# Kernel optimization log

Measured on AMD Instinct MI355X. Metric: run time of the kernel, lower is better.

Reference implementation:

```python
import jax, jax.numpy as jnp
import numpy as np

N_NODES = 20000
N_EDGES = 600000
HIDDEN = 128
OUT = 128
EPS = 0.0  # GINConv default eps, not trainable by default


def _mlp(x, W1, b1, W2, b2):
    h = jax.nn.relu(x @ W1 + b1)
    return jax.nn.relu(h @ W2 + b2)


def _gin_conv(x, edge_index, W1, b1, W2, b2):
    src, dst = edge_index[0], edge_index[1]
    # scatter-add neighbor aggregation: agg[dst] += x[src]
    agg = jax.ops.segment_sum(x[src], dst, num_segments=N_NODES)
    return _mlp((1.0 + EPS) * x + agg, W1, b1, W2, b2)


def _forward_once(x, edge_index, params):
    (W11, b11, W12, b12, W21, b21, W22, b22, Wf, bf) = params
    x = _gin_conv(x, edge_index, W11, b11, W12, b12)
    x = _gin_conv(x, edge_index, W21, b21, W22, b22)
    g = jnp.sum(x, axis=0)  # sum-pool over nodes -> [HIDDEN]
    return g @ Wf + bf


def setup_inputs() -> dict:
    key = jax.random.key(0)
    ks = jax.random.split(key, 16)
    def lin(k, fan_in, fan_out):
        kw, kb = jax.random.split(k)
        bound = 1.0 / np.sqrt(fan_in)
        W = jax.random.uniform(kw, (fan_in, fan_out), jnp.float32, -bound, bound)
        b = jax.random.uniform(kb, (fan_out,), jnp.float32, -bound, bound)
        return W, b
    W11, b11 = lin(ks[0], 1, HIDDEN)
    W12, b12 = lin(ks[1], HIDDEN, HIDDEN)
    W21, b21 = lin(ks[2], HIDDEN, HIDDEN)
    W22, b22 = lin(ks[3], HIDDEN, HIDDEN)
    Wf, bf = lin(ks[4], HIDDEN, OUT)
    inp = {
        "x_a": jax.random.normal(ks[5], (N_NODES, 1), jnp.float32),
        "edge_index_a": jax.random.randint(ks[6], (2, N_EDGES), 0, N_NODES, jnp.int64 if jax.config.jax_enable_x64 else jnp.int32),
        "x_p": jax.random.normal(ks[7], (N_NODES, 1), jnp.float32),
        "edge_index_p": jax.random.randint(ks[8], (2, N_EDGES), 0, N_NODES, jnp.int64 if jax.config.jax_enable_x64 else jnp.int32),
        "x_n": jax.random.normal(ks[9], (N_NODES, 1), jnp.float32),
        "edge_index_n": jax.random.randint(ks[10], (2, N_EDGES), 0, N_NODES, jnp.int64 if jax.config.jax_enable_x64 else jnp.int32),
        "W11": W11, "b11": b11, "W12": W12, "b12": b12,
        "W21": W21, "b21": b21, "W22": W22, "b22": b22,
        "Wf": Wf, "bf": bf,
    }
    return inp


def reference(x_a, edge_index_a, x_p, edge_index_p, x_n, edge_index_n,
              W11, b11, W12, b12, W21, b21, W22, b22, Wf, bf):
    params = (W11, b11, W12, b12, W21, b21, W22, b22, Wf, bf)
    a = _forward_once(x_a, edge_index_a, params)
    p = _forward_once(x_p, edge_index_p, params)
    n = _forward_once(x_n, edge_index_n, params)
    return (a, p, n)
```

## Files before the change

### kernel.cpp

```cpp
#include <hip/hip_runtime.h>

#define N_NODES 20000
#define N_EDGES 600000
#define HID 128
#define NB N_NODES
#define NBP (NB + 8)
#define NBLK64 313
#define BPG 160
#define CHUNK (N_EDGES / BPG)
#define NBUCK 157
#define BSH 7
#define COLCAP 760832

typedef unsigned int uint32;
typedef __attribute__((ext_vector_type(8))) short bf16x8v;
typedef __attribute__((ext_vector_type(4))) float f32x4;
typedef __attribute__((ext_vector_type(2))) float f32x2;

#define P_OFF     0
#define BCNT_OFF  1800000
#define BBASE_OFF 1875360
#define X1_OFF    1875840
#define H2_OFF    5717376
#define COL_OFF   9557376
#define RPE_OFF   11839872
#define GSUM_OFF  11959872
#define TS_OFF    11960256
#define UV_OFF    11960384
#define W21P_OFF  11993408
#define W22P_OFF  12001600

static __device__ inline unsigned short f2bf(float f) {
    uint32 u = __float_as_uint(f);
    return (unsigned short)((u + 0x7fffu + ((u >> 16) & 1u)) >> 16);
}
static __device__ inline uint32 pack2(float a, float b) {
    return (uint32)f2bf(a) | ((uint32)f2bf(b) << 16);
}
static __device__ inline f32x2 unpk(uint32 v) {
    f32x2 r;
    r.x = __uint_as_float(v << 16);
    r.y = __uint_as_float(v & 0xffff0000u);
    return r;
}

__launch_bounds__(256)
__global__ void prep2_kernel(const float* __restrict__ W11, const float* __restrict__ b11,
                             const float* __restrict__ W12, const float* __restrict__ b12,
                             const float* __restrict__ W21, const float* __restrict__ W22,
                             float* __restrict__ ts, float* __restrict__ UV,
                             uint32* __restrict__ W21p, uint32* __restrict__ W22p,
                             float* __restrict__ gsum) {
    int blk = blockIdx.x, tid = threadIdx.x;
    if (blk < 8) {
        __shared__ float w12s[128][16];
        __shared__ float du[128][16];
        __shared__ float dv[128][16];
        __shared__ float pu[16][16], pv[16][16];
        __shared__ float bu[16][16], bv[16][16];
        __shared__ float wsh[128], bsh[128], tss[128], tsh[128];
        __shared__ int osh[128];
        int c0 = blk * 16;
        if (tid < 128) {
            float w = W11[tid], b = b11[tid];
            wsh[tid] = w; bsh[tid] = b;
            tsh[tid] = (w != 0.0f) ? (-b / w) : 3.0e38f;
        }
        {
            int r0 = tid >> 4, cc2 = tid & 15;
            for (int r = r0; r < 128; r += 16)
                w12s[r][cc2] = W12[r * HID + c0 + cc2];
        }
        __syncthreads();
        if (tid < 128) {
            float t = tsh[tid];
            int rank = 0;
            for (int j = 0; j < 128; ++j) {
                float tj = tsh[j];
                if (tj < t || (tj == t && j < tid)) ++rank;
            }
            tss[rank] = t; osh[rank] = tid;
        }
        __syncthreads();
        if (blk == 0 && tid < 128) ts[tid] = tss[tid];
        int c = tid & 15, t = tid >> 4;
        float su = 0.f, sv = 0.f;
#pragma unroll
        for (int m = 0; m < 8; ++m) {
            int j = t * 8 + m;
            int k = osh[j];
            float wk = wsh[k], bk = bsh[k], w12 = w12s[k][c];
            float sg = (wk > 0.f) ? 1.f : ((wk < 0.f) ? -1.f : 0.f);
            du[j][c] = sg * wk * w12;
            dv[j][c] = sg * bk * w12;
            float wb = wsh[j], bb = bsh[j], w12b = w12s[j][c];
            if (wb < 0.f)                     { su += wb * w12b; sv += bb * w12b; }
            else if (wb == 0.f && bb > 0.f)   { sv += bb * w12b; }
        }
        bu[t][c] = su; bv[t][c] = sv;
        __syncthreads();
        float ru = 0.f, rv = 0.f;
#pragma unroll
        for (int m = 0; m < 8; ++m) {
            int j = t * 8 + m;
            ru += du[j][c]; du[j][c] = ru;
            rv += dv[j][c]; dv[j][c] = rv;
        }
        pu[t][c] = ru; pv[t][c] = rv;
        __syncthreads();
        if (t == 0) {
            float baseu = 0.f;
            float basev = b12[c0 + c];
            for (int q = 0; q < 16; ++q) { baseu += bu[q][c]; basev += bv[q][c]; }
            float ou = baseu, ov = basev;
            for (int q = 0; q < 16; ++q) {
                float tu = pu[q][c], tv = pv[q][c];
                pu[q][c] = ou; pv[q][c] = ov;
                ou += tu; ov += tv;
            }
            UV[c0 + c] = baseu; UV[128 + c0 + c] = basev;
        }
        __syncthreads();
        float offu = pu[t][c], offv = pv[t][c];
#pragma unroll
        for (int m = 0; m < 8; ++m) {
            int j = t * 8 + m;
            UV[(j + 1) * 256 + c0 + c]       = offu + du[j][c];
            UV[(j + 1) * 256 + 128 + c0 + c] = offv + dv[j][c];
        }
    } else {
        int idx = (blk - 8) * 256 + tid;
        int tt = idx >> 9, c = (idx >> 6) & 7, l = idx & 63;
        int kbase = tt * 32 + (l >> 4) * 8;
        int colv = c * 16 + (l & 15);
#pragma unroll
        for (int jw = 0; jw < 4; ++jw) {
            float f0 = W21[(kbase + 2 * jw) * HID + colv];
            float f1 = W21[(kbase + 2 * jw + 1) * HID + colv];
            W21p[idx * 4 + jw] = pack2(f0, f1);
            f0 = W22[(kbase + 2 * jw) * HID + colv];
            f1 = W22[(kbase + 2 * jw + 1) * HID + colv];
            W22p[idx * 4 + jw] = pack2(f0, f1);
        }
        if (blk == 8)
            for (int i = tid; i < 384; i += 256) gsum[i] = 0.0f;
    }
}

__launch_bounds__(512)
__global__ void bhist_kernel(const int* __restrict__ ea, const int* __restrict__ ep,
                             const int* __restrict__ en, uint32* __restrict__ bcnt) {
    __shared__ uint32 c[NBUCK];
    int g = blockIdx.y, blk = blockIdx.x, tid = threadIdx.x;
    const int* e = (g == 0) ? ea : (g == 1) ? ep : en;
    if (tid < NBUCK) c[tid] = 0;
    __syncthreads();
    int base = blk * CHUNK;
    for (int i = tid; i < CHUNK; i += 512)
        atomicAdd(&c[e[N_EDGES + base + i] >> BSH], 1u);
    __syncthreads();
    if (tid < NBUCK) bcnt[((size_t)g * BPG + blk) * NBUCK + tid] = c[tid];
}

__launch_bounds__(256)
__global__ void bscan_kernel(uint32* __restrict__ bcnt, uint32* __restrict__ bbase) {
    __shared__ uint32 btot[NBUCK];
    int g = blockIdx.x, tid = threadIdx.x;
    if (tid < NBUCK) {
        uint32 run = 0;
        for (int blk = 0; blk < BPG; ++blk) {
            size_t idx = ((size_t)g * BPG + blk) * NBUCK + tid;
            uint32 t = bcnt[idx];
            bcnt[idx] = run;
            run += t;
        }
        btot[tid] = run;
    }
    __syncthreads();
    if (tid == 0) {
        uint32 run = 0;
        for (int k = 0; k < NBUCK; ++k) { bbase[g * 158 + k] = run; run += btot[k]; }
        bbase[g * 158 + NBUCK] = run;
    }
}

__launch_bounds__(512)
__global__ void bpart_kernel(const int* __restrict__ ea, const int* __restrict__ ep,
                             const int* __restrict__ en, const uint32* __restrict__ bcnt,
                             const uint32* __restrict__ bbase, uint32* __restrict__ P) {
    __shared__ uint32 cur[NBUCK];
    int g = blockIdx.y, blk = blockIdx.x, tid = threadIdx.x;
    const int* e = (g == 0) ? ea : (g == 1) ? ep : en;
    if (tid < NBUCK)
        cur[tid] = bbase[g * 158 + tid] + bcnt[((size_t)g * BPG + blk) * NBUCK + tid];
    __syncthreads();
    int base = blk * CHUNK;
    uint32* Pg = P + (size_t)g * N_EDGES;
    for (int i = tid; i < CHUNK; i += 512) {
        int src = e[base + i];
        int dst = e[N_EDGES + base + i];
        uint32 pos = atomicAdd(&cur[dst >> BSH], 1u);
        Pg[pos] = (uint32)src | ((uint32)(dst & 127) << 16);
    }
}

__launch_bounds__(256)
__global__ void bcsr_l1_kernel(const uint32* __restrict__ bbase, const uint32* __restrict__ P,
                               const float* __restrict__ xa, const float* __restrict__ xp,
                               const float* __restrict__ xn,
                               const float* __restrict__ ts, const float* __restrict__ UV,
                               int* __restrict__ rpe, uint32* __restrict__ col,
                               uint32* __restrict__ X1) {
    __shared__ uint32 h[128];
    __shared__ uint32 hraw[128];
    __shared__ uint32 pls[128];
    __shared__ uint32 wendS;
    __shared__ float accs[128];
    __shared__ float tsh[128];
    __shared__ int pat[128];
    int k = blockIdx.x, g = blockIdx.y, tid = threadIdx.x;
    const float* x = (g == 0) ? xa : (g == 1) ? xp : xn;
    int beg = (int)bbase[g * 158 + k], end = (int)bbase[g * 158 + k + 1];
    int size = end - beg;
    int wbase = beg + k * 1024;
    int n0 = k * 128;
    int cnt_nodes = NB - n0; if (cnt_nodes > 128) cnt_nodes = 128;
    const uint32 ZOFFB = (uint32)NB << 8;
    if (tid < 128) { h[tid] = 0; accs[tid] = 0.0f; tsh[tid] = ts[tid]; }
    __syncthreads();
    const uint32* Pg = P + (size_t)g * N_EDGES + beg;
    for (int i = tid; i < size; i += 256)
        atomicAdd(&h[(Pg[i] >> 16) & 127], 1u);
    __syncthreads();
    if (tid == 0) {
        uint32 run = 0;
        for (int d = 0; d < 128; ++d) {
            hraw[d] = h[d];
            pls[d] = run;
            run += (h[d] + 8u) & ~7u;
        }
        wendS = (uint32)wbase + run;
    }
    __syncthreads();
    uint32* colg = col + (size_t)g * COLCAP;
    if (tid < cnt_nodes) {
        int node = n0 + tid;
        rpe[((size_t)g * NB + node) * 2]     = wbase + (int)pls[tid];
        rpe[((size_t)g * NB + node) * 2 + 1] = wbase + (int)(pls[tid] + ((hraw[tid] + 8u) & ~7u));
        colg[wbase + pls[tid]] = (uint32)node << 8;
        uint32 e0 = pls[tid] + 1u + hraw[tid];
        uint32 e1 = pls[tid] + ((hraw[tid] + 8u) & ~7u);
        for (uint32 q = e0; q < e1; ++q) colg[wbase + q] = ZOFFB;
    } else if (tid < 128) {
        uint32 e0 = pls[tid];
        uint32 e1 = pls[tid] + 8u;
        for (uint32 q = e0; q < e1; ++q) colg[wbase + q] = ZOFFB;
    }
    if (tid < 128) h[tid] = pls[tid] + 1u;
    __syncthreads();
    for (int i = tid; i < size; i += 256) {
        uint32 w = Pg[i];
        int d = (w >> 16) & 127;
        int src = (int)(w & 0xffffu);
        uint32 r = atomicAdd(&h[d], 1u);
        colg[wbase + r] = (uint32)src << 8;
        atomicAdd(&accs[d], x[src]);
    }
    if (k == 0 && tid < 64)
        *((uint32*)&X1[((size_t)g * NBP + NB) * 64] + tid) = 0u;
    if (k == NBUCK - 1 && tid < 64)
        colg[wendS + tid] = ZOFFB;
    __syncthreads();
    if (tid < cnt_nodes) {
        float s = accs[tid] + x[n0 + tid];
        int lo = 0, hi = 128;
        while (lo < hi) { int mid = (lo + hi) >> 1; if (tsh[mid] < s) lo = mid + 1; else hi = mid; }
        pat[tid] = lo;
        accs[tid] = s;
    }
    __syncthreads();
    uint32* X1g = X1 + ((size_t)g * NBP + n0) * 64;
#pragma unroll 4
    for (int it = 0; it < 32; ++it) {
        int idx = it * 256 + tid;
        int d = idx >> 6, w = idx & 63;
        if (d < cnt_nodes) {
            const float* Up = UV + (size_t)pat[d] * 256;
            float s = accs[d];
            float2 u = *(const float2*)&Up[w * 2];
            float2 v = *(const float2*)&Up[128 + w * 2];
            float r0 = fmaxf(fmaf(s, u.x, v.x), 0.0f);
            float r1 = fmaxf(fmaf(s, u.y, v.y), 0.0f);
            X1g[(size_t)d * 64 + w] = pack2(r0, r1);
        }
    }
}

__launch_bounds__(256)
__global__ void gather2_kernel(const int* __restrict__ rpe, const uint32* __restrict__ col,
                               const uint32* __restrict__ X1, uint32* __restrict__ H2) {
    int b = blockIdx.x;
    int xcd = b & 7, s = b >> 3;
    int phase = s / 313, slot = s - phase * 313;
    const int gt[3][2] = {{0, 1}, {2, 2}, {0, 1}};
    const int ht[3][2] = {{0, 0}, {0, 1}, {1, 1}};
    int g = gt[phase][xcd >> 2];
    int h = ht[phase][xcd >> 2];
    int nb = slot * 4 + (xcd & 3);
    if (nb >= 1250) return;
    int tid = threadIdx.x;
    int wave = tid >> 6, lane = tid & 63;
    int node = nb * 16 + wave * 4 + (lane >> 4);
    int l4 = lane & 15;
    int sl = l4 >> 3;
    int w = l4 & 7;
    const uint32* colg = col + (size_t)g * COLCAP;
    int2 be = *(const int2*)&rpe[((size_t)g * NB + node) * 2];
    int beg = be.x, end = be.y;
    const char* Bg = (const char*)(X1 + (size_t)g * NBP * 64) + h * 128 + w * 16;
    f32x2 A0 = {0.f, 0.f}, A1 = {0.f, 0.f}, A2 = {0.f, 0.f}, A3 = {0.f, 0.f};
    uint32 ca = colg[beg + sl];
    uint32 cb = colg[beg + 2 + sl];
    uint32 cc = colg[beg + 4 + sl];
    uint32 cd = colg[beg + 6 + sl];
    for (int j = beg; j < end; j += 8) {
        uint32 c0 = ca, c1 = cb, c2 = cc, c3 = cd;
        ca = colg[j + 8 + sl];
        cb = colg[j + 10 + sl];
        cc = colg[j + 12 + sl];
        cd = colg[j + 14 + sl];
        uint4 v0 = *(const uint4*)(Bg + c0);
        uint4 v1 = *(const uint4*)(Bg + c1);
        uint4 v2 = *(const uint4*)(Bg + c2);
        uint4 v3 = *(const uint4*)(Bg + c3);
        A0 += unpk(v0.x); A1 += unpk(v0.y); A2 += unpk(v0.z); A3 += unpk(v0.w);
        A0 += unpk(v1.x); A1 += unpk(v1.y); A2 += unpk(v1.z); A3 += unpk(v1.w);
        A0 += unpk(v2.x); A1 += unpk(v2.y); A2 += unpk(v2.z); A3 += unpk(v2.w);
        A0 += unpk(v3.x); A1 += unpk(v3.y); A2 += unpk(v3.z); A3 += unpk(v3.w);
    }
    float a0 = A0.x, a1 = A0.y, a2 = A1.x, a3 = A1.y;
    float a4 = A2.x, a5 = A2.y, a6 = A3.x, a7 = A3.y;
    a0 += __shfl_xor(a0, 8);
    a1 += __shfl_xor(a1, 8);
    a2 += __shfl_xor(a2, 8);
    a3 += __shfl_xor(a3, 8);
    a4 += __shfl_xor(a4, 8);
    a5 += __shfl_xor(a5, 8);
    a6 += __shfl_xor(a6, 8);
    a7 += __shfl_xor(a7, 8);
    if (sl == 0) {
        uint4 o;
        o.x = pack2(a0, a1); o.y = pack2(a2, a3);
        o.z = pack2(a4, a5); o.w = pack2(a6, a7);
        *(uint4*)&H2[(size_t)(g * NB + node) * 64 + h * 32 + w * 4] = o;
    }
}

__launch_bounds__(256)
__global__ void mlp2_kernel(const uint32* __restrict__ H2,
                            const uint32* __restrict__ W21p, const float* __restrict__ b21,
                            const uint32* __restrict__ W22p, const float* __restrict__ b22,
                            float* __restrict__ gsum) {
    __shared__ uint32 tl[64 * 64];
    __shared__ float psum[HID];
    int g = blockIdx.y;
    int base = blockIdx.x * 64;
    int nvalid = NB - base; if (nvalid > 64) nvalid = 64;
    int tid = threadIdx.x;
    int wave = tid >> 6, l = tid & 63;
    int lq = l >> 4, lr = l & 15;
    if (tid < HID) psum[tid] = 0.0f;
    __syncthreads();

    f32x4 acc[8];
#pragma unroll
    for (int c = 0; c < 8; ++c) acc[c] = (f32x4){0.f, 0.f, 0.f, 0.f};
    int arow = wave * 16 + lr;
    int arowc = (arow < nvalid) ? arow : 0;
    const uint32* h2row = H2 + ((size_t)g * NB + base + arowc) * 64;
#pragma unroll
    for (int t = 0; t < 4; ++t) {
        uint4 av = *(const uint4*)&h2row[t * 16 + lq * 4];
        bf16x8v af = __builtin_bit_cast(bf16x8v, av);
#pragma unroll
        for (int c = 0; c < 8; ++c) {
            uint4 bv = *(const uint4*)&W21p[((t * 8 + c) * 64 + l) * 4];
            acc[c] = __builtin_amdgcn_mfma_f32_16x16x32_bf16(
                af, __builtin_bit_cast(bf16x8v, bv), acc[c], 0, 0, 0);
        }
    }
    unsigned short* tls = (unsigned short*)tl;
#pragma unroll
    for (int c = 0; c < 8; ++c) {
        int colv = c * 16 + lr;
        float bb = b21[colv];
#pragma unroll
        for (int q = 0; q < 4; ++q) {
            int row = wave * 16 + lq * 4 + q;
            float v = fmaxf(acc[c][q] + bb, 0.0f);
            int byte = row * 256 + ((colv * 2) ^ ((row & 7) << 4));
            tls[byte >> 1] = f2bf(v);
        }
    }
    f32x4 acc2[8];
#pragma unroll
    for (int c = 0; c < 8; ++c) acc2[c] = (f32x4){0.f, 0.f, 0.f, 0.f};
#pragma unroll
    for (int t = 0; t < 4; ++t) {
        int rbyte = arow * 256 + (((t * 64 + lq * 16)) ^ ((arow & 7) << 4));
        uint4 av = *(const uint4*)((const char*)tl + rbyte);
        bf16x8v af = __builtin_bit_cast(bf16x8v, av);
#pragma unroll
        for (int c = 0; c < 8; ++c) {
            uint4 bv = *(const uint4*)&W22p[((t * 8 + c) * 64 + l) * 4];
            acc2[c] = __builtin_amdgcn_mfma_f32_16x16x32_bf16(
                af, __builtin_bit_cast(bf16x8v, bv), acc2[c], 0, 0, 0);
        }
    }
#pragma unroll
    for (int c = 0; c < 8; ++c) {
        float bb = b22[c * 16 + lr];
        float s = 0.0f;
#pragma unroll
        for (int q = 0; q < 4; ++q) {
            int row = wave * 16 + lq * 4 + q;
            float v = fmaxf(acc2[c][q] + bb, 0.0f);
            s += (row < nvalid) ? v : 0.0f;
        }
        s += __shfl_xor(s, 16);
        s += __shfl_xor(s, 32);
        if (lq == 0) atomicAdd(&psum[c * 16 + lr], s);
    }
    __syncthreads();
    if (tid < HID) atomicAdd(&gsum[g * HID + tid], psum[tid]);
}

__global__ void final_kernel(const float* __restrict__ gsum, const float* __restrict__ Wf,
                             const float* __restrict__ bf, float* __restrict__ out) {
    int tid = threadIdx.x;
    int g = tid >> 7;
    int o = tid & 127;
    float acc = bf[o];
    for (int k = 0; k < HID; ++k)
        acc += gsum[g * HID + k] * Wf[k * HID + o];
    out[g * HID + o] = acc;
}

extern "C" void kernel_launch(void* const* d_in, const int* in_sizes, int n_in,
                              void* d_out, int out_size, void* d_ws, size_t ws_size,
                              hipStream_t stream) {
    const float* xa = (const float*)d_in[0];
    const int*   ea = (const int*)d_in[1];
    const float* xp = (const float*)d_in[2];
    const int*   ep = (const int*)d_in[3];
    const float* xn = (const float*)d_in[4];
    const int*   en = (const int*)d_in[5];
    const float* W11 = (const float*)d_in[6];
    const float* b11 = (const float*)d_in[7];
    const float* W12 = (const float*)d_in[8];
    const float* b12 = (const float*)d_in[9];
    const float* W21 = (const float*)d_in[10];
    const float* b21 = (const float*)d_in[11];
    const float* W22 = (const float*)d_in[12];
    const float* b22 = (const float*)d_in[13];
    const float* Wf  = (const float*)d_in[14];
    const float* bf  = (const float*)d_in[15];

    float*  ws    = (float*)d_ws;
    uint32* P     = (uint32*)(ws + P_OFF);
    uint32* bcnt  = (uint32*)(ws + BCNT_OFF);
    uint32* bbase = (uint32*)(ws + BBASE_OFF);
    uint32* X1    = (uint32*)(ws + X1_OFF);
    uint32* H2    = (uint32*)(ws + H2_OFF);
    uint32* col   = (uint32*)(ws + COL_OFF);
    int*    rpe   = (int*)(ws + RPE_OFF);
    float*  gsum  = ws + GSUM_OFF;
    float*  ts    = ws + TS_OFF;
    float*  UV    = ws + UV_OFF;
    uint32* W21p  = (uint32*)(ws + W21P_OFF);
    uint32* W22p  = (uint32*)(ws + W22P_OFF);
    float*  out   = (float*)d_out;

    prep2_kernel<<<16, 256, 0, stream>>>(W11, b11, W12, b12, W21, W22, ts, UV, W21p, W22p, gsum);
    bhist_kernel<<<dim3(BPG, 3), 512, 0, stream>>>(ea, ep, en, bcnt);
    bscan_kernel<<<3, 256, 0, stream>>>(bcnt, bbase);
    bpart_kernel<<<dim3(BPG, 3), 512, 0, stream>>>(ea, ep, en, bcnt, bbase, P);
    bcsr_l1_kernel<<<dim3(NBUCK, 3), 256, 0, stream>>>(bbase, P, xa, xp, xn, ts, UV, rpe, col, X1);
    gather2_kernel<<<7512, 256, 0, stream>>>(rpe, col, X1, H2);
    mlp2_kernel<<<dim3(NBLK64, 3), 256, 0, stream>>>(H2, W21p, b21, W22p, b22, gsum);
    final_kernel<<<1, 384, 0, stream>>>(gsum, Wf, bf, out);
}
```

Before: 133.1 us.

## Merge prep into histogram kernel and fold bucket scan into partition kernel

The weight-prep work now runs as extra blocks inside the bucket-histogram launch. The separate scan kernel is removed: every partition block recomputes its own prefix offsets and the bucket totals from the histogram counts. This cuts the launch count from eight to six and removes two serial launch gaps. In exchange, each of the 480 partition blocks re-reads all 160 count rows for its graph, and the prep blocks carry a larger 512-thread shape in which half the threads sit idle.

```diff
diff --git a/kernel.cpp b/kernel.cpp
--- a/kernel.cpp
+++ b/kernel.cpp
@@ -44,15 +44,32 @@
     return r;
 }
 
-__launch_bounds__(256)
-__global__ void prep2_kernel(const float* __restrict__ W11, const float* __restrict__ b11,
-                             const float* __restrict__ W12, const float* __restrict__ b12,
-                             const float* __restrict__ W21, const float* __restrict__ W22,
-                             float* __restrict__ ts, float* __restrict__ UV,
-                             uint32* __restrict__ W21p, uint32* __restrict__ W22p,
-                             float* __restrict__ gsum) {
-    int blk = blockIdx.x, tid = threadIdx.x;
-    if (blk < 8) {
+__launch_bounds__(512)
+__global__ void bhist_prep_kernel(const int* __restrict__ ea, const int* __restrict__ ep,
+                                  const int* __restrict__ en, uint32* __restrict__ bcnt,
+                                  const float* __restrict__ W11, const float* __restrict__ b11,
+                                  const float* __restrict__ W12, const float* __restrict__ b12,
+                                  const float* __restrict__ W21, const float* __restrict__ W22,
+                                  float* __restrict__ ts, float* __restrict__ UV,
+                                  uint32* __restrict__ W21p, uint32* __restrict__ W22p,
+                                  float* __restrict__ gsum) {
+    int tid = threadIdx.x;
+    if (blockIdx.x < BPG) {
+        __shared__ uint32 c[NBUCK];
+        int g = blockIdx.y, blk = blockIdx.x;
+        const int* e = (g == 0) ? ea : (g == 1) ? ep : en;
+        if (tid < NBUCK) c[tid] = 0;
+        __syncthreads();
+        int base = blk * CHUNK;
+        for (int i = tid; i < CHUNK; i += 512)
+            atomicAdd(&c[e[N_EDGES + base + i] >> BSH], 1u);
+        __syncthreads();
+        if (tid < NBUCK) bcnt[((size_t)g * BPG + blk) * NBUCK + tid] = c[tid];
+        return;
+    }
+    int p = (blockIdx.x - BPG) * 3 + blockIdx.y;
+    if (p >= 16) return;
+    if (p < 8) {
         __shared__ float w12s[128][16];
         __shared__ float du[128][16];
         __shared__ float dv[128][16];
@@ -60,7 +77,7 @@
         __shared__ float bu[16][16], bv[16][16];
         __shared__ float wsh[128], bsh[128], tss[128], tsh[128];
         __shared__ int osh[128];
-        int c0 = blk * 16;
+        int c0 = p * 16;
         if (tid < 128) {
             float w = W11[tid], b = b11[tid];
             wsh[tid] = w; bsh[tid] = b;
@@ -68,7 +85,7 @@
         }
         {
             int r0 = tid >> 4, cc2 = tid & 15;
-            for (int r = r0; r < 128; r += 16)
+            for (int r = r0; r < 128; r += 32)
                 w12s[r][cc2] = W12[r * HID + c0 + cc2];
         }
         __syncthreads();
@@ -82,31 +99,35 @@
             tss[rank] = t; osh[rank] = tid;
         }
         __syncthreads();
-        if (blk == 0 && tid < 128) ts[tid] = tss[tid];
+        if (p == 0 && tid < 128) ts[tid] = tss[tid];
         int c = tid & 15, t = tid >> 4;
-        float su = 0.f, sv = 0.f;
-#pragma unroll
-        for (int m = 0; m < 8; ++m) {
-            int j = t * 8 + m;
-            int k = osh[j];
-            float wk = wsh[k], bk = bsh[k], w12 = w12s[k][c];
-            float sg = (wk > 0.f) ? 1.f : ((wk < 0.f) ? -1.f : 0.f);
-            du[j][c] = sg * wk * w12;
-            dv[j][c] = sg * bk * w12;
-            float wb = wsh[j], bb = bsh[j], w12b = w12s[j][c];
-            if (wb < 0.f)                     { su += wb * w12b; sv += bb * w12b; }
-            else if (wb == 0.f && bb > 0.f)   { sv += bb * w12b; }
-        }
-        bu[t][c] = su; bv[t][c] = sv;
-        __syncthreads();
-        float ru = 0.f, rv = 0.f;
-#pragma unroll
-        for (int m = 0; m < 8; ++m) {
-            int j = t * 8 + m;
-            ru += du[j][c]; du[j][c] = ru;
-            rv += dv[j][c]; dv[j][c] = rv;
-        }
-        pu[t][c] = ru; pv[t][c] = rv;
+        if (t < 16) {
+            float su = 0.f, sv = 0.f;
+#pragma unroll
+            for (int m = 0; m < 8; ++m) {
+                int j = t * 8 + m;
+                int k = osh[j];
+                float wk = wsh[k], bk = bsh[k], w12 = w12s[k][c];
+                float sg = (wk > 0.f) ? 1.f : ((wk < 0.f) ? -1.f : 0.f);
+                du[j][c] = sg * wk * w12;
+                dv[j][c] = sg * bk * w12;
+                float wb = wsh[j], bb = bsh[j], w12b = w12s[j][c];
+                if (wb < 0.f)                     { su += wb * w12b; sv += bb * w12b; }
+                else if (wb == 0.f && bb > 0.f)   { sv += bb * w12b; }
+            }
+            bu[t][c] = su; bv[t][c] = sv;
+        }
+        __syncthreads();
+        if (t < 16) {
+            float ru = 0.f, rv = 0.f;
+#pragma unroll
+            for (int m = 0; m < 8; ++m) {
+                int j = t * 8 + m;
+                ru += du[j][c]; du[j][c] = ru;
+                rv += dv[j][c]; dv[j][c] = rv;
+            }
+            pu[t][c] = ru; pv[t][c] = rv;
+        }
         __syncthreads();
         if (t == 0) {
             float baseu = 0.f;
@@ -121,15 +142,17 @@
             UV[c0 + c] = baseu; UV[128 + c0 + c] = basev;
         }
         __syncthreads();
-        float offu = pu[t][c], offv = pv[t][c];
-#pragma unroll
-        for (int m = 0; m < 8; ++m) {
-            int j = t * 8 + m;
-            UV[(j + 1) * 256 + c0 + c]       = offu + du[j][c];
-            UV[(j + 1) * 256 + 128 + c0 + c] = offv + dv[j][c];
-        }
-    } else {
-        int idx = (blk - 8) * 256 + tid;
+        if (t < 16) {
+            float offu = pu[t][c], offv = pv[t][c];
+#pragma unroll
+            for (int m = 0; m < 8; ++m) {
+                int j = t * 8 + m;
+                UV[(j + 1) * 256 + c0 + c]       = offu + du[j][c];
+                UV[(j + 1) * 256 + 128 + c0 + c] = offv + dv[j][c];
+            }
+        }
+    } else if (tid < 256) {
+        int idx = (p - 8) * 256 + tid;
         int tt = idx >> 9, c = (idx >> 6) & 7, l = idx & 63;
         int kbase = tt * 32 + (l >> 4) * 8;
         int colv = c * 16 + (l & 15);
@@ -142,57 +165,40 @@
             f1 = W22[(kbase + 2 * jw + 1) * HID + colv];
             W22p[idx * 4 + jw] = pack2(f0, f1);
         }
-        if (blk == 8)
+        if (p == 8)
             for (int i = tid; i < 384; i += 256) gsum[i] = 0.0f;
-    }
-}
-
-__launch_bounds__(512)
-__global__ void bhist_kernel(const int* __restrict__ ea, const int* __restrict__ ep,
-                             const int* __restrict__ en, uint32* __restrict__ bcnt) {
-    __shared__ uint32 c[NBUCK];
-    int g = blockIdx.y, blk = blockIdx.x, tid = threadIdx.x;
-    const int* e = (g == 0) ? ea : (g == 1) ? ep : en;
-    if (tid < NBUCK) c[tid] = 0;
-    __syncthreads();
-    int base = blk * CHUNK;
-    for (int i = tid; i < CHUNK; i += 512)
-        atomicAdd(&c[e[N_EDGES + base + i] >> BSH], 1u);
-    __syncthreads();
-    if (tid < NBUCK) bcnt[((size_t)g * BPG + blk) * NBUCK + tid] = c[tid];
-}
-
-__launch_bounds__(256)
-__global__ void bscan_kernel(uint32* __restrict__ bcnt, uint32* __restrict__ bbase) {
-    __shared__ uint32 btot[NBUCK];
-    int g = blockIdx.x, tid = threadIdx.x;
-    if (tid < NBUCK) {
-        uint32 run = 0;
-        for (int blk = 0; blk < BPG; ++blk) {
-            size_t idx = ((size_t)g * BPG + blk) * NBUCK + tid;
-            uint32 t = bcnt[idx];
-            bcnt[idx] = run;
-            run += t;
-        }
-        btot[tid] = run;
-    }
-    __syncthreads();
-    if (tid == 0) {
-        uint32 run = 0;
-        for (int k = 0; k < NBUCK; ++k) { bbase[g * 158 + k] = run; run += btot[k]; }
-        bbase[g * 158 + NBUCK] = run;
     }
 }
 
 __launch_bounds__(512)
 __global__ void bpart_kernel(const int* __restrict__ ea, const int* __restrict__ ep,
                              const int* __restrict__ en, const uint32* __restrict__ bcnt,
-                             const uint32* __restrict__ bbase, uint32* __restrict__ P) {
+                             uint32* __restrict__ bbase, uint32* __restrict__ P) {
     __shared__ uint32 cur[NBUCK];
+    __shared__ uint32 totS[NBUCK];
+    __shared__ uint32 sbase[NBUCK + 1];
     int g = blockIdx.y, blk = blockIdx.x, tid = threadIdx.x;
     const int* e = (g == 0) ? ea : (g == 1) ? ep : en;
-    if (tid < NBUCK)
-        cur[tid] = bbase[g * 158 + tid] + bcnt[((size_t)g * BPG + blk) * NBUCK + tid];
+    if (tid < NBUCK) {
+        uint32 myoff = 0, tot = 0;
+        const uint32* bc = bcnt + (size_t)g * BPG * NBUCK + tid;
+        for (int k = 0; k < BPG; ++k) {
+            uint32 v = bc[(size_t)k * NBUCK];
+            if (k < blk) myoff += v;
+            tot += v;
+        }
+        cur[tid] = myoff;
+        totS[tid] = tot;
+    }
+    __syncthreads();
+    if (tid == 0) {
+        uint32 run = 0;
+        for (int b2 = 0; b2 < NBUCK; ++b2) { sbase[b2] = run; run += totS[b2]; }
+        sbase[NBUCK] = run;
+    }
+    __syncthreads();
+    if (tid < NBUCK) cur[tid] += sbase[tid];
+    if (blk == 0 && tid <= NBUCK) bbase[g * 158 + tid] = sbase[tid];
     __syncthreads();
     int base = blk * CHUNK;
     uint32* Pg = P + (size_t)g * N_EDGES;
@@ -481,9 +487,8 @@
     uint32* W22p  = (uint32*)(ws + W22P_OFF);
     float*  out   = (float*)d_out;
 
-    prep2_kernel<<<16, 256, 0, stream>>>(W11, b11, W12, b12, W21, W22, ts, UV, W21p, W22p, gsum);
-    bhist_kernel<<<dim3(BPG, 3), 512, 0, stream>>>(ea, ep, en, bcnt);
-    bscan_kernel<<<3, 256, 0, stream>>>(bcnt, bbase);
+    bhist_prep_kernel<<<dim3(BPG + 6, 3), 512, 0, stream>>>(
+        ea, ep, en, bcnt, W11, b11, W12, b12, W21, W22, ts, UV, W21p, W22p, gsum);
     bpart_kernel<<<dim3(BPG, 3), 512, 0, stream>>>(ea, ep, en, bcnt, bbase, P);
     bcsr_l1_kernel<<<dim3(NBUCK, 3), 256, 0, stream>>>(bbase, P, xa, xp, xn, ts, UV, rpe, col, X1);
     gather2_kernel<<<7512, 256, 0, stream>>>(rpe, col, X1, H2);
```

Result: faster. 125.7 us (median of 2 runs) (-5.6%).
